# Kernel optimization log

Measured on AMD Instinct MI355X. Metric: run time of the kernel, lower is better.

## Reference

```python
import jax, jax.numpy as jnp
import numpy as np

ALPHA = 0.2  # LeakyReLU negative slope
NEG_INF = -9e15


def setup_inputs() -> dict:
    key = jax.random.key(0)
    k1, k2, k3, k4 = jax.random.split(key, 4)
    N, IN_F, OUT_F, H = 8192, 256, 128, 2
    HD = OUT_F // H
    h = jax.random.normal(k1, (N, IN_F), dtype=jnp.float32)
    adj = jax.random.randint(k2, (N, N), 0, 2, dtype=jnp.int32)
    # xavier_uniform with gain=1.414
    g = 1.414
    limW = g * np.sqrt(6.0 / (IN_F + HD))
    W = jax.random.uniform(k3, (H, IN_F, HD), jnp.float32, -limW, limW)
    lima = g * np.sqrt(6.0 / (2 * HD + 1))
    a = jax.random.uniform(k4, (H, 2 * HD, 1), jnp.float32, -lima, lima)
    return {"h": h, "adj": adj, "W": W, "a": a}


def reference(h, adj, W, a):
    # Wh: (H, N, HD)
    Wh = jnp.einsum('ni,hid->hnd', h, W)
    HD = W.shape[-1]
    a1 = a[:, :HD, 0]   # (H, HD) -> applied to Wh_i
    a2 = a[:, HD:, 0]   # (H, HD) -> applied to Wh_j
    # a . [Wh_i || Wh_j] == a1.Wh_i + a2.Wh_j ; avoids the (N,N,2HD) tensor
    f1 = jnp.einsum('hnd,hd->hn', Wh, a1)  # (H, N)
    f2 = jnp.einsum('hnd,hd->hn', Wh, a2)  # (H, N)
    e = jax.nn.leaky_relu(f1[:, :, None] + f2[:, None, :], ALPHA)  # (H, N, N)
    mask = (adj > 0)[None, :, :]
    e = jnp.where(mask, e, NEG_INF)
    attention = jax.nn.softmax(e, axis=-1)  # (H, N, N)
    # dropout is identity in eval mode
    h_prime = jnp.einsum('hnm,hmd->hnd', attention, Wh)  # (H, N, HD)
    N = h.shape[0]
    h_prime = jnp.transpose(h_prime, (1, 0, 2)).reshape(N, -1)  # concat heads
    return jax.nn.elu(h_prime)
```

## Files before the change

kernel.cpp:

```cpp
#include <hip/hip_runtime.h>
#include <hip/hip_bf16.h>
#include <stdint.h>

#define N_NODES 8192
#define IN_F    256
#define HD      64
#define NH      2
#define MS      8
#define SLICE   1024
#define NT      16
#define ALPHA   0.2f

typedef __attribute__((ext_vector_type(8))) short bf16x8s;
typedef __attribute__((ext_vector_type(4))) float f32x4;

#define OFF_U      0
#define OFF_WFRAG  4096
#define OFF_F1     69632
#define OFF_F2     135168
#define OFF_F2MAX  200704
#define OFF_G2     200960
#define OFF_WHB    332032
#define OFF_OP     2429184
#define OFF_LP     35983616

__device__ __forceinline__ unsigned short f2bf(float x) {
  union { float f; uint32_t u; } c; c.f = x;
  uint32_t r = c.u + 0x7FFFu + ((c.u >> 16) & 1u);
  return (unsigned short)(r >> 16);
}
__device__ __forceinline__ short f2bfs(float x) {
  __hip_bfloat16 b = __float2bfloat16(x);
  return __builtin_bit_cast(short, b);
}

__global__ void gat_prep_kernel(const float* __restrict__ W, const float* __restrict__ a,
                                float* __restrict__ u, unsigned short* __restrict__ wfrag)
{
  int idx = blockIdx.x * 256 + threadIdx.x;
  if (idx < 32768) {
    int j = idx & 7, lane = (idx >> 3) & 63, ks = (idx >> 9) & 7, Dt = idx >> 12;
    int k  = ks * 32 + ((lane >> 4) << 3) + j;
    int dp = Dt * 16 + (lane & 15);
    int hh = dp >> 6, d = dp & 63;
    wfrag[idx] = f2bf(W[(size_t)(hh * IN_F + k) * HD + d]);
  } else if (idx < 32768 + NH * 2 * IN_F) {
    int i2 = idx - 32768;
    int i = i2 & 255, v = (i2 >> 8) & 1, h = i2 >> 9;
    const float* Wp = W + (size_t)(h * IN_F + i) * HD;
    const float* ap = a + h * 2 * HD + v * HD;
    float s = 0.f;
    for (int d = 0; d < HD; ++d) s += Wp[d] * ap[d];
    u[(h * 2 + v) * IN_F + i] = s;
  }
}

__global__ __launch_bounds__(256) void gat_f12_kernel(const float* __restrict__ hmat,
    const float* __restrict__ u, float* __restrict__ f1, float* __restrict__ f2,
    uint32_t* __restrict__ g2b)
{
  int n = blockIdx.x * 4 + (threadIdx.x >> 6);
  int l = threadIdx.x & 63;
  float4 hv = *(const float4*)(hmat + (size_t)n * IN_F + l * 4);
  float s[4];
#pragma unroll
  for (int q = 0; q < 4; ++q) {
    float4 uv = *(const float4*)(u + q * IN_F + l * 4);
    s[q] = hv.x * uv.x + hv.y * uv.y + hv.z * uv.z + hv.w * uv.w;
  }
#pragma unroll
  for (int off = 1; off < 64; off <<= 1) {
#pragma unroll
    for (int q = 0; q < 4; ++q) s[q] += __shfl_xor(s[q], off);
  }
  if (l == 0) {
    f1[n] = s[0];           f2[n] = s[1];
    f1[N_NODES + n] = s[2]; f2[N_NODES + n] = s[3];
    g2b[n]           = (uint32_t)f2bf(__expf(s[1])) | ((uint32_t)f2bf(__expf(ALPHA * s[1])) << 16);
    g2b[N_NODES + n] = (uint32_t)f2bf(__expf(s[3])) | ((uint32_t)f2bf(__expf(ALPHA * s[3])) << 16);
  }
}

__global__ void gat_f2max_kernel(const float* __restrict__ f2, float* __restrict__ f2m)
{
  int h = blockIdx.x;
  float m = -1e30f;
  for (int i = threadIdx.x; i < N_NODES; i += 256) m = fmaxf(m, f2[h * N_NODES + i]);
#pragma unroll
  for (int off = 1; off < 64; off <<= 1) m = fmaxf(m, __shfl_xor(m, off));
  __shared__ float red[4];
  if ((threadIdx.x & 63) == 0) red[threadIdx.x >> 6] = m;
  __syncthreads();
  if (threadIdx.x == 0) f2m[h] = fmaxf(fmaxf(red[0], red[1]), fmaxf(red[2], red[3]));
}

__global__ __launch_bounds__(256) void gat_wh_kernel(const float* __restrict__ hmat,
    const unsigned short* __restrict__ wfrag, unsigned short* __restrict__ whb)
{
  int tid = threadIdx.x;
  int w = tid >> 6, l = tid & 63;
  int n0 = blockIdx.x * 64;
  int row = n0 + w * 16 + (l & 15);
  f32x4 acc[8] = {};
#pragma unroll
  for (int ks = 0; ks < 8; ++ks) {
    const float* ap = hmat + (size_t)row * IN_F + ks * 32 + ((l >> 4) << 3);
    float av[8];
    *(float4*)&av[0] = *(const float4*)ap;
    *(float4*)&av[4] = *(const float4*)(ap + 4);
    bf16x8s af;
#pragma unroll
    for (int j = 0; j < 8; ++j) af[j] = f2bfs(av[j]);
#pragma unroll
    for (int Dt = 0; Dt < 8; ++Dt) {
      bf16x8s bfv = *(const bf16x8s*)(wfrag + ((size_t)(Dt * 8 + ks) * 64 + l) * 8);
      acc[Dt] = __builtin_amdgcn_mfma_f32_16x16x32_bf16(af, bfv, acc[Dt], 0, 0, 0);
    }
  }
  int Tm = blockIdx.x;
  int s  = w >> 1;
  int lb = ((w & 1) * 2 + ((l >> 4) >> 1)) * 16 + (l & 15);
  int jh = (l >> 4) & 1;
#pragma unroll
  for (int Dt = 0; Dt < 8; ++Dt) {
    int hh = Dt >> 2, D = Dt & 3;
    ushort4 pk;
    pk.x = f2bf(acc[Dt][0]); pk.y = f2bf(acc[Dt][1]);
    pk.z = f2bf(acc[Dt][2]); pk.w = f2bf(acc[Dt][3]);
    size_t off = ((((size_t)(hh * 128 + Tm) * 2 + s) * 4 + D) * 64 + lb) * 8 + jh * 4;
    *(ushort4*)(whb + off) = pk;
  }
}

__global__ __launch_bounds__(256, 4) void gat_attn_kernel(
    const int* __restrict__ adj, const unsigned short* __restrict__ whb,
    const float* __restrict__ f1, const uint32_t* __restrict__ g2b,
    const float* __restrict__ f2max, float* __restrict__ Opart, float* __restrict__ Lpart)
{
  int bx = blockIdx.x;
  int split = bx & (MS - 1);
  int T = bx >> 3;
  int tid = threadIdx.x;
  int w = tid >> 6, l = tid & 63;
  int n0 = T * 64;
  int row = n0 + w * 16 + (l & 15);
  int mbase = split * SLICE;
  int koff = (l >> 4) << 3;
  int cb = mbase >> 6;

  __shared__ uint32_t glp[2][SLICE];
  __shared__ uint4 wbuf[2][1024];

  {
    const uint4* s0 = (const uint4*)(g2b + mbase);
    const uint4* s1 = (const uint4*)(g2b + N_NODES + mbase);
    ((uint4*)glp[0])[tid] = s0[tid];
    ((uint4*)glp[1])[tid] = s1[tid];
  }

  float E1[NH], Ea[NH];
#pragma unroll
  for (int h = 0; h < NH; ++h) {
    float f1v = f1[h * N_NODES + row];
    float tm  = f1v + f2max[h];
    float mrow = fmaxf(tm, ALPHA * tm);
    E1[h] = __expf(f1v - mrow);
    Ea[h] = __expf(ALPHA * f1v - mrow);
  }

  const int* ap = adj + (size_t)row * N_NODES + mbase + koff;
  const uint4* wsrc = (const uint4*)whb;

  uint4 rw0, rw1, rw2, rw3;
  {
    const uint4* w0 = wsrc + (size_t)cb * 512;
    const uint4* w1 = wsrc + (size_t)(128 + cb) * 512;
    rw0 = w0[tid]; rw1 = w0[tid + 256]; rw2 = w1[tid]; rw3 = w1[tid + 256];
  }
  int4 c0 = *(const int4*)(ap);      int4 c1 = *(const int4*)(ap + 4);
  int4 c2 = *(const int4*)(ap + 32); int4 c3 = *(const int4*)(ap + 36);
  wbuf[0][tid]       = rw0; wbuf[0][tid + 256] = rw1;
  wbuf[0][tid + 512] = rw2; wbuf[0][tid + 768] = rw3;
  __syncthreads();

  f32x4 acc[NH][4] = {};
  float lsum[NH] = {0.f, 0.f};

  for (int mt = 0; mt < NT; ++mt) {
    int p = mt & 1;
    if (mt + 1 < NT) {
      const uint4* w0 = wsrc + (size_t)(cb + mt + 1) * 512;
      const uint4* w1 = wsrc + (size_t)(128 + cb + mt + 1) * 512;
      rw0 = w0[tid]; rw1 = w0[tid + 256]; rw2 = w1[tid]; rw3 = w1[tid + 256];
    }

    bf16x8s af[NH][2];
#pragma unroll
    for (int s = 0; s < 2; ++s) {
      int aj[8];
      if (s == 0) { *(int4*)&aj[0] = c0; *(int4*)&aj[4] = c1; }
      else        { *(int4*)&aj[0] = c2; *(int4*)&aj[4] = c3; }
      uint32_t gv[NH][8];
#pragma unroll
      for (int h = 0; h < NH; ++h) {
        const uint4* gp = (const uint4*)&glp[h][mt * 64 + s * 32 + koff];
        *(uint4*)&gv[h][0] = gp[0];
        *(uint4*)&gv[h][4] = gp[1];
      }
#pragma unroll
      for (int h = 0; h < NH; ++h) {
        float ps = 0.f;
#pragma unroll
        for (int j = 0; j < 8; ++j) {
          uint32_t uv = gv[h][j];
          float g1 = __builtin_bit_cast(float, uv << 16);
          float ga = __builtin_bit_cast(float, uv & 0xffff0000u);
          float v  = fmaxf(E1[h] * g1, Ea[h] * ga);
          float pz = (aj[j] > 0) ? v : 0.f;
          ps += pz;
          af[h][s][j] = f2bfs(pz);
        }
        lsum[h] += ps;
      }
      if (mt + 1 < NT) {
        const int* apn = ap + (mt + 1) * 64;
        if (s == 0) { c0 = *(const int4*)(apn);      c1 = *(const int4*)(apn + 4); }
        else        { c2 = *(const int4*)(apn + 32); c3 = *(const int4*)(apn + 36); }
      }
    }

    const unsigned short* lb = (const unsigned short*)wbuf[p];
#pragma unroll
    for (int h = 0; h < NH; ++h)
#pragma unroll
      for (int s = 0; s < 2; ++s)
#pragma unroll
        for (int D = 0; D < 4; ++D) {
          bf16x8s bfv = *(const bf16x8s*)&lb[(h * 8 + s * 4 + D) * 512 + l * 8];
          acc[h][D] = __builtin_amdgcn_mfma_f32_16x16x32_bf16(af[h][s], bfv, acc[h][D], 0, 0, 0);
        }

    if (mt + 1 < NT) {
      wbuf[p ^ 1][tid]       = rw0; wbuf[p ^ 1][tid + 256] = rw1;
      wbuf[p ^ 1][tid + 512] = rw2; wbuf[p ^ 1][tid + 768] = rw3;
    }
    __syncthreads();
  }

#pragma unroll
  for (int h = 0; h < NH; ++h) {
    float ls = lsum[h];
    ls += __shfl_xor(ls, 16);
    ls += __shfl_xor(ls, 32);
    if (l < 16) Lpart[((size_t)(split * NH + h) << 13) + n0 + w * 16 + l] = ls;
    float* op = Opart + (size_t)(split * NH + h) * N_NODES * HD;
#pragma unroll
    for (int D = 0; D < 4; ++D)
#pragma unroll
      for (int r = 0; r < 4; ++r) {
        int orow = n0 + w * 16 + ((l >> 4) << 2) + r;
        op[(size_t)orow * HD + D * 16 + (l & 15)] = acc[h][D][r];
      }
  }
}

__global__ __launch_bounds__(256) void gat_final_kernel(const float* __restrict__ Opart,
    const float* __restrict__ Lpart, float* __restrict__ out)
{
  int idx = blockIdx.x * 256 + threadIdx.x;
  int n = idx >> 7, c = idx & 127;
  int h = c >> 6, d = c & 63;
  float v = 0.f, ls = 0.f;
#pragma unroll
  for (int sp = 0; sp < MS; ++sp) {
    v  += Opart[((size_t)(sp * NH + h) * N_NODES + n) * HD + d];
    ls += Lpart[(size_t)(sp * NH + h) * N_NODES + n];
  }
  float r = v / fmaxf(ls, 1e-30f);
  out[idx] = (r > 0.f) ? r : (__expf(r) - 1.f);
}

extern "C" void kernel_launch(void* const* d_in, const int* in_sizes, int n_in,
                              void* d_out, int out_size, void* d_ws, size_t ws_size,
                              hipStream_t stream)
{
  const float* hmat = (const float*)d_in[0];
  const int*   adj  = (const int*)d_in[1];
  const float* W    = (const float*)d_in[2];
  const float* a    = (const float*)d_in[3];
  float* out = (float*)d_out;
  char* ws = (char*)d_ws;

  float* u             = (float*)(ws + OFF_U);
  unsigned short* wfrg = (unsigned short*)(ws + OFF_WFRAG);
  float* f1            = (float*)(ws + OFF_F1);
  float* f2            = (float*)(ws + OFF_F2);
  float* f2m           = (float*)(ws + OFF_F2MAX);
  uint32_t* g2b        = (uint32_t*)(ws + OFF_G2);
  unsigned short* whb  = (unsigned short*)(ws + OFF_WHB);
  float* Opart         = (float*)(ws + OFF_OP);
  float* Lpart         = (float*)(ws + OFF_LP);

  gat_prep_kernel <<<132, 256, 0, stream>>>(W, a, u, wfrg);
  gat_f12_kernel  <<<N_NODES / 4, 256, 0, stream>>>(hmat, u, f1, f2, g2b);
  gat_f2max_kernel<<<NH, 256, 0, stream>>>(f2, f2m);
  gat_wh_kernel   <<<N_NODES / 64, 256, 0, stream>>>(hmat, wfrg, whb);
  gat_attn_kernel <<<128 * MS, 256, 0, stream>>>(adj, whb, f1, g2b, f2m, Opart, Lpart);
  gat_final_kernel<<<out_size / 256, 256, 0, stream>>>(Opart, Lpart, out);
}
```

Before: 113.2 us.

## Stage Wh tiles via direct global-to-LDS loads with triple buffering

```diff
diff --git a/kernel.cpp b/kernel.cpp
--- a/kernel.cpp
+++ b/kernel.cpp
@@ -13,6 +13,8 @@
 
 typedef __attribute__((ext_vector_type(8))) short bf16x8s;
 typedef __attribute__((ext_vector_type(4))) float f32x4;
+typedef __attribute__((address_space(3))) uint32_t lds_u32_t;
+typedef const __attribute__((address_space(1))) uint32_t gbl_u32_t;
 
 #define OFF_U      0
 #define OFF_WFRAG  4096
@@ -132,7 +134,7 @@
   }
 }
 
-__global__ __launch_bounds__(256, 4) void gat_attn_kernel(
+__global__ __launch_bounds__(256, 2) void gat_attn_kernel(
     const int* __restrict__ adj, const unsigned short* __restrict__ whb,
     const float* __restrict__ f1, const uint32_t* __restrict__ g2b,
     const float* __restrict__ f2max, float* __restrict__ Opart, float* __restrict__ Lpart)
@@ -149,7 +151,7 @@
   int cb = mbase >> 6;
 
   __shared__ uint32_t glp[2][SLICE];
-  __shared__ uint4 wbuf[2][1024];
+  __shared__ uint4 wbuf[3][1024];
 
   {
     const uint4* s0 = (const uint4*)(g2b + mbase);
@@ -168,51 +170,57 @@
     Ea[h] = __expf(ALPHA * f1v - mrow);
   }
 
+  __syncthreads();
+
   const int* ap = adj + (size_t)row * N_NODES + mbase + koff;
   const uint4* wsrc = (const uint4*)whb;
 
-  uint4 rw0, rw1, rw2, rw3;
-  {
-    const uint4* w0 = wsrc + (size_t)cb * 512;
-    const uint4* w1 = wsrc + (size_t)(128 + cb) * 512;
-    rw0 = w0[tid]; rw1 = w0[tid + 256]; rw2 = w1[tid]; rw3 = w1[tid + 256];
-  }
-  int4 c0 = *(const int4*)(ap);      int4 c1 = *(const int4*)(ap + 4);
-  int4 c2 = *(const int4*)(ap + 32); int4 c3 = *(const int4*)(ap + 36);
-  wbuf[0][tid]       = rw0; wbuf[0][tid + 256] = rw1;
-  wbuf[0][tid + 512] = rw2; wbuf[0][tid + 768] = rw3;
-  __syncthreads();
+  auto stage = [&](int tile, int bufi) {
+    const uint4* gsb = (w < 2)
+        ? (wsrc + (size_t)(cb + tile) * 512 + w * 256)
+        : (wsrc + (size_t)(128 + cb + tile) * 512 + (w - 2) * 256);
+    char* lb = (char*)&wbuf[0][0] + bufi * 16384 + w * 4096;
+#pragma unroll
+    for (int k = 0; k < 4; ++k) {
+      __builtin_amdgcn_global_load_lds((gbl_u32_t*)(gsb + k * 64 + l),
+                                       (lds_u32_t*)(lb + k * 1024), 16, 0, 0);
+    }
+  };
+  auto ldadj = [&](int tile, int4* c) {
+    const int* p = ap + tile * 64;
+    c[0] = *(const int4*)p;        c[1] = *(const int4*)(p + 4);
+    c[2] = *(const int4*)(p + 32); c[3] = *(const int4*)(p + 36);
+  };
+
+  int4 cE[4], cO[4];
+  stage(0, 0); ldadj(0, cE);
+  stage(1, 1); ldadj(1, cO);
 
   f32x4 acc[NH][4] = {};
   float lsum[NH] = {0.f, 0.f};
 
-  for (int mt = 0; mt < NT; ++mt) {
-    int p = mt & 1;
-    if (mt + 1 < NT) {
-      const uint4* w0 = wsrc + (size_t)(cb + mt + 1) * 512;
-      const uint4* w1 = wsrc + (size_t)(128 + cb + mt + 1) * 512;
-      rw0 = w0[tid]; rw1 = w0[tid + 256]; rw2 = w1[tid]; rw3 = w1[tid + 256];
-    }
+  auto body = [&](int mt, int4* cc) {
+    if (mt < NT - 1) asm volatile("s_waitcnt vmcnt(8)" ::: "memory");
+    else             asm volatile("s_waitcnt vmcnt(0)" ::: "memory");
+    __builtin_amdgcn_s_barrier();
+
+    int cur = mt % 3;
 
     bf16x8s af[NH][2];
 #pragma unroll
     for (int s = 0; s < 2; ++s) {
       int aj[8];
-      if (s == 0) { *(int4*)&aj[0] = c0; *(int4*)&aj[4] = c1; }
-      else        { *(int4*)&aj[0] = c2; *(int4*)&aj[4] = c3; }
-      uint32_t gv[NH][8];
+      *(int4*)&aj[0] = cc[2 * s]; *(int4*)&aj[4] = cc[2 * s + 1];
 #pragma unroll
       for (int h = 0; h < NH; ++h) {
         const uint4* gp = (const uint4*)&glp[h][mt * 64 + s * 32 + koff];
-        *(uint4*)&gv[h][0] = gp[0];
-        *(uint4*)&gv[h][4] = gp[1];
-      }
-#pragma unroll
-      for (int h = 0; h < NH; ++h) {
+        uint32_t gv[8];
+        *(uint4*)&gv[0] = gp[0];
+        *(uint4*)&gv[4] = gp[1];
         float ps = 0.f;
 #pragma unroll
         for (int j = 0; j < 8; ++j) {
-          uint32_t uv = gv[h][j];
+          uint32_t uv = gv[j];
           float g1 = __builtin_bit_cast(float, uv << 16);
           float ga = __builtin_bit_cast(float, uv & 0xffff0000u);
           float v  = fmaxf(E1[h] * g1, Ea[h] * ga);
@@ -222,14 +230,14 @@
         }
         lsum[h] += ps;
       }
-      if (mt + 1 < NT) {
-        const int* apn = ap + (mt + 1) * 64;
-        if (s == 0) { c0 = *(const int4*)(apn);      c1 = *(const int4*)(apn + 4); }
-        else        { c2 = *(const int4*)(apn + 32); c3 = *(const int4*)(apn + 36); }
-      }
     }
 
-    const unsigned short* lb = (const unsigned short*)wbuf[p];
+    if (mt + 2 < NT) {
+      stage(mt + 2, (mt + 2) % 3);
+      ldadj(mt + 2, cc);
+    }
+
+    const unsigned short* lb = (const unsigned short*)wbuf + (size_t)cur * 8192;
 #pragma unroll
     for (int h = 0; h < NH; ++h)
 #pragma unroll
@@ -239,12 +247,11 @@
           bf16x8s bfv = *(const bf16x8s*)&lb[(h * 8 + s * 4 + D) * 512 + l * 8];
           acc[h][D] = __builtin_amdgcn_mfma_f32_16x16x32_bf16(af[h][s], bfv, acc[h][D], 0, 0, 0);
         }
-
-    if (mt + 1 < NT) {
-      wbuf[p ^ 1][tid]       = rw0; wbuf[p ^ 1][tid + 256] = rw1;
-      wbuf[p ^ 1][tid + 512] = rw2; wbuf[p ^ 1][tid + 768] = rw3;
-    }
-    __syncthreads();
+  };
+
+  for (int mt = 0; mt < NT; mt += 2) {
+    body(mt, cE);
+    body(mt + 1, cO);
   }
 
 #pragma unroll
```

Result: slower. 118.3 us (+4.5%).

## Bitpack adjacency in LDS, split columns across waves, fuse final reduction

Applied to the files above, without the earlier changes.

```diff
diff --git a/kernel.cpp b/kernel.cpp
--- a/kernel.cpp
+++ b/kernel.cpp
@@ -6,9 +6,7 @@
 #define IN_F    256
 #define HD      64
 #define NH      2
-#define MS      8
-#define SLICE   1024
-#define NT      16
+#define BROWS   32
 #define ALPHA   0.2f
 
 typedef __attribute__((ext_vector_type(8))) short bf16x8s;
@@ -21,8 +19,6 @@
 #define OFF_F2MAX  200704
 #define OFF_G2     200960
 #define OFF_WHB    332032
-#define OFF_OP     2429184
-#define OFF_LP     35983616
 
 __device__ __forceinline__ unsigned short f2bf(float x) {
   union { float f; uint32_t u; } c; c.f = x;
@@ -132,152 +128,172 @@
   }
 }
 
-__global__ __launch_bounds__(256, 4) void gat_attn_kernel(
+__global__ __launch_bounds__(512, 2) void gat_attn_kernel(
     const int* __restrict__ adj, const unsigned short* __restrict__ whb,
     const float* __restrict__ f1, const uint32_t* __restrict__ g2b,
-    const float* __restrict__ f2max, float* __restrict__ Opart, float* __restrict__ Lpart)
-{
-  int bx = blockIdx.x;
-  int split = bx & (MS - 1);
-  int T = bx >> 3;
+    const float* __restrict__ f2max, float* __restrict__ out)
+{
+  __shared__ unsigned long long maskbuf[BROWS][128];
+  __shared__ uint32_t glp[2][N_NODES];
+  __shared__ float redbuf[12288];
+  __shared__ float lsumbuf[8][2][16];
+
   int tid = threadIdx.x;
-  int w = tid >> 6, l = tid & 63;
-  int n0 = T * 64;
-  int row = n0 + w * 16 + (l & 15);
-  int mbase = split * SLICE;
+  int wv = tid >> 6, l = tid & 63;
+  int rb = blockIdx.x * BROWS;
+
+  {
+    uint4* gd = (uint4*)glp;
+    const uint4* gs = (const uint4*)g2b;
+#pragma unroll
+    for (int i = 0; i < 8; ++i) gd[i * 512 + tid] = gs[i * 512 + tid];
+  }
+
+#pragma unroll 1
+  for (int r = 0; r < 4; ++r) {
+    int lrow = wv * 4 + r;
+    const int4* src = (const int4*)(adj + (size_t)(rb + lrow) * N_NODES) + l;
+#pragma unroll 1
+    for (int cc = 0; cc < 4; ++cc) {
+      int4 v[8];
+#pragma unroll
+      for (int u2 = 0; u2 < 8; ++u2) v[u2] = src[(cc * 8 + u2) * 64];
+#pragma unroll
+      for (int u2 = 0; u2 < 8; ++u2) {
+        int c = cc * 8 + u2;
+        unsigned long long b0 = __ballot(v[u2].x > 0);
+        unsigned long long b1 = __ballot(v[u2].y > 0);
+        unsigned long long b2 = __ballot(v[u2].z > 0);
+        unsigned long long b3 = __ballot(v[u2].w > 0);
+        if (l == 0) {
+          ulonglong2* mp = (ulonglong2*)&maskbuf[lrow][c * 4];
+          mp[0] = make_ulonglong2(b0, b1);
+          mp[1] = make_ulonglong2(b2, b3);
+        }
+      }
+    }
+  }
+  __syncthreads();
+
+  int h = wv & 1, q = wv >> 1;
+  int mtbase = q * 32;
   int koff = (l >> 4) << 3;
-  int cb = mbase >> 6;
-
-  __shared__ uint32_t glp[2][SLICE];
-  __shared__ uint4 wbuf[2][1024];
-
-  {
-    const uint4* s0 = (const uint4*)(g2b + mbase);
-    const uint4* s1 = (const uint4*)(g2b + N_NODES + mbase);
-    ((uint4*)glp[0])[tid] = s0[tid];
-    ((uint4*)glp[1])[tid] = s1[tid];
-  }
-
-  float E1[NH], Ea[NH];
-#pragma unroll
-  for (int h = 0; h < NH; ++h) {
-    float f1v = f1[h * N_NODES + row];
+
+  float E1v[2], Eav[2];
+#pragma unroll
+  for (int rg = 0; rg < 2; ++rg) {
+    float f1v = f1[h * N_NODES + rb + rg * 16 + (l & 15)];
     float tm  = f1v + f2max[h];
     float mrow = fmaxf(tm, ALPHA * tm);
-    E1[h] = __expf(f1v - mrow);
-    Ea[h] = __expf(ALPHA * f1v - mrow);
-  }
-
-  const int* ap = adj + (size_t)row * N_NODES + mbase + koff;
-  const uint4* wsrc = (const uint4*)whb;
-
-  uint4 rw0, rw1, rw2, rw3;
-  {
-    const uint4* w0 = wsrc + (size_t)cb * 512;
-    const uint4* w1 = wsrc + (size_t)(128 + cb) * 512;
-    rw0 = w0[tid]; rw1 = w0[tid + 256]; rw2 = w1[tid]; rw3 = w1[tid + 256];
-  }
-  int4 c0 = *(const int4*)(ap);      int4 c1 = *(const int4*)(ap + 4);
-  int4 c2 = *(const int4*)(ap + 32); int4 c3 = *(const int4*)(ap + 36);
-  wbuf[0][tid]       = rw0; wbuf[0][tid + 256] = rw1;
-  wbuf[0][tid + 512] = rw2; wbuf[0][tid + 768] = rw3;
-  __syncthreads();
-
-  f32x4 acc[NH][4] = {};
-  float lsum[NH] = {0.f, 0.f};
-
-  for (int mt = 0; mt < NT; ++mt) {
-    int p = mt & 1;
-    if (mt + 1 < NT) {
-      const uint4* w0 = wsrc + (size_t)(cb + mt + 1) * 512;
-      const uint4* w1 = wsrc + (size_t)(128 + cb + mt + 1) * 512;
-      rw0 = w0[tid]; rw1 = w0[tid + 256]; rw2 = w1[tid]; rw3 = w1[tid + 256];
-    }
-
-    bf16x8s af[NH][2];
+    E1v[rg] = __expf(f1v - mrow);
+    Eav[rg] = __expf(ALPHA * f1v - mrow);
+  }
+
+  const uint4* wp = (const uint4*)whb + ((size_t)(h * 128 + mtbase) * 8) * 64 + l;
+
+  f32x4 acc[2][4] = {};
+  float lsum[2] = {0.f, 0.f};
+  unsigned long long cm[2][4];
+  uint4 cur[8], nxt[8];
+#pragma unroll
+  for (int i = 0; i < 8; ++i) cur[i] = wp[i * 64];
+
+#pragma unroll 2
+  for (int t = 0; t < 32; ++t) {
+    int mt = mtbase + t;
+    if ((t & 3) == 0) {
+      int cidx = (mt >> 2) * 4;
+      ulonglong2 m00 = *(const ulonglong2*)&maskbuf[l & 15][cidx];
+      ulonglong2 m01 = *(const ulonglong2*)&maskbuf[l & 15][cidx + 2];
+      ulonglong2 m10 = *(const ulonglong2*)&maskbuf[16 + (l & 15)][cidx];
+      ulonglong2 m11 = *(const ulonglong2*)&maskbuf[16 + (l & 15)][cidx + 2];
+      cm[0][0] = m00.x; cm[0][1] = m00.y; cm[0][2] = m01.x; cm[0][3] = m01.y;
+      cm[1][0] = m10.x; cm[1][1] = m10.y; cm[1][2] = m11.x; cm[1][3] = m11.y;
+    }
+    if (t + 1 < 32) {
+      const uint4* p = wp + (size_t)(t + 1) * 512;
+#pragma unroll
+      for (int i = 0; i < 8; ++i) nxt[i] = p[i * 64];
+    }
+
+    bf16x8s af[2][2];
 #pragma unroll
     for (int s = 0; s < 2; ++s) {
-      int aj[8];
-      if (s == 0) { *(int4*)&aj[0] = c0; *(int4*)&aj[4] = c1; }
-      else        { *(int4*)&aj[0] = c2; *(int4*)&aj[4] = c3; }
-      uint32_t gv[NH][8];
-#pragma unroll
-      for (int h = 0; h < NH; ++h) {
-        const uint4* gp = (const uint4*)&glp[h][mt * 64 + s * 32 + koff];
-        *(uint4*)&gv[h][0] = gp[0];
-        *(uint4*)&gv[h][4] = gp[1];
-      }
-#pragma unroll
-      for (int h = 0; h < NH; ++h) {
+      int sh = ((mt & 3) << 4) + (s << 3) + ((l >> 4) << 1);
+      const uint4* gp = (const uint4*)&glp[h][(mt << 6) + s * 32 + koff];
+      uint32_t gv[8];
+      *(uint4*)&gv[0] = gp[0];
+      *(uint4*)&gv[4] = gp[1];
+#pragma unroll
+      for (int rg = 0; rg < 2; ++rg) {
+        uint32_t b0 = (uint32_t)(cm[rg][0] >> sh), b1 = (uint32_t)(cm[rg][1] >> sh);
+        uint32_t b2 = (uint32_t)(cm[rg][2] >> sh), b3 = (uint32_t)(cm[rg][3] >> sh);
         float ps = 0.f;
 #pragma unroll
         for (int j = 0; j < 8; ++j) {
-          uint32_t uv = gv[h][j];
+          uint32_t uv = gv[j];
           float g1 = __builtin_bit_cast(float, uv << 16);
           float ga = __builtin_bit_cast(float, uv & 0xffff0000u);
-          float v  = fmaxf(E1[h] * g1, Ea[h] * ga);
-          float pz = (aj[j] > 0) ? v : 0.f;
-          ps += pz;
-          af[h][s][j] = f2bfs(pz);
+          float v  = fmaxf(E1v[rg] * g1, Eav[rg] * ga);
+          uint32_t bb = (j & 3) == 0 ? b0 : (j & 3) == 1 ? b1 : (j & 3) == 2 ? b2 : b3;
+          float p = ((bb >> (j >> 2)) & 1) ? v : 0.f;
+          ps += p;
+          af[rg][s][j] = f2bfs(p);
         }
-        lsum[h] += ps;
+        lsum[rg] += ps;
       }
-      if (mt + 1 < NT) {
-        const int* apn = ap + (mt + 1) * 64;
-        if (s == 0) { c0 = *(const int4*)(apn);      c1 = *(const int4*)(apn + 4); }
-        else        { c2 = *(const int4*)(apn + 32); c3 = *(const int4*)(apn + 36); }
+    }
+
+#pragma unroll
+    for (int s = 0; s < 2; ++s)
+#pragma unroll
+      for (int D = 0; D < 4; ++D) {
+        bf16x8s bfv = __builtin_bit_cast(bf16x8s, cur[s * 4 + D]);
+        acc[0][D] = __builtin_amdgcn_mfma_f32_16x16x32_bf16(af[0][s], bfv, acc[0][D], 0, 0, 0);
+        acc[1][D] = __builtin_amdgcn_mfma_f32_16x16x32_bf16(af[1][s], bfv, acc[1][D], 0, 0, 0);
       }
-    }
-
-    const unsigned short* lb = (const unsigned short*)wbuf[p];
-#pragma unroll
-    for (int h = 0; h < NH; ++h)
-#pragma unroll
-      for (int s = 0; s < 2; ++s)
-#pragma unroll
-        for (int D = 0; D < 4; ++D) {
-          bf16x8s bfv = *(const bf16x8s*)&lb[(h * 8 + s * 4 + D) * 512 + l * 8];
-          acc[h][D] = __builtin_amdgcn_mfma_f32_16x16x32_bf16(af[h][s], bfv, acc[h][D], 0, 0, 0);
-        }
-
-    if (mt + 1 < NT) {
-      wbuf[p ^ 1][tid]       = rw0; wbuf[p ^ 1][tid + 256] = rw1;
-      wbuf[p ^ 1][tid + 512] = rw2; wbuf[p ^ 1][tid + 768] = rw3;
-    }
-    __syncthreads();
-  }
-
-#pragma unroll
-  for (int h = 0; h < NH; ++h) {
-    float ls = lsum[h];
+#pragma unroll
+    for (int i = 0; i < 8; ++i) cur[i] = nxt[i];
+  }
+
+#pragma unroll
+  for (int rg = 0; rg < 2; ++rg) {
+    float ls = lsum[rg];
     ls += __shfl_xor(ls, 16);
     ls += __shfl_xor(ls, 32);
-    if (l < 16) Lpart[((size_t)(split * NH + h) << 13) + n0 + w * 16 + l] = ls;
-    float* op = Opart + (size_t)(split * NH + h) * N_NODES * HD;
-#pragma unroll
-    for (int D = 0; D < 4; ++D)
-#pragma unroll
-      for (int r = 0; r < 4; ++r) {
-        int orow = n0 + w * 16 + ((l >> 4) << 2) + r;
-        op[(size_t)orow * HD + D * 16 + (l & 15)] = acc[h][D][r];
-      }
-  }
-}
-
-__global__ __launch_bounds__(256) void gat_final_kernel(const float* __restrict__ Opart,
-    const float* __restrict__ Lpart, float* __restrict__ out)
-{
-  int idx = blockIdx.x * 256 + threadIdx.x;
-  int n = idx >> 7, c = idx & 127;
-  int h = c >> 6, d = c & 63;
-  float v = 0.f, ls = 0.f;
-#pragma unroll
-  for (int sp = 0; sp < MS; ++sp) {
-    v  += Opart[((size_t)(sp * NH + h) * N_NODES + n) * HD + d];
-    ls += Lpart[(size_t)(sp * NH + h) * N_NODES + n];
-  }
-  float r = v / fmaxf(ls, 1e-30f);
-  out[idx] = (r > 0.f) ? r : (__expf(r) - 1.f);
+    if (l < 16) lsumbuf[wv][rg][l] = ls;
+  }
+  __syncthreads();
+
+  if (q > 0) {
+    float* rp = &redbuf[(h * 3 + (q - 1)) * 2048];
+#pragma unroll
+    for (int rg = 0; rg < 2; ++rg)
+#pragma unroll
+      for (int D = 0; D < 4; ++D)
+#pragma unroll
+        for (int r = 0; r < 4; ++r)
+          rp[rg * 1024 + D * 256 + ((l >> 4) * 4 + r) * 16 + (l & 15)] = acc[rg][D][r];
+  }
+  __syncthreads();
+  if (q == 0) {
+    const float* rp = &redbuf[h * 3 * 2048];
+#pragma unroll
+    for (int rg = 0; rg < 2; ++rg)
+#pragma unroll
+      for (int D = 0; D < 4; ++D)
+#pragma unroll
+        for (int r = 0; r < 4; ++r) {
+          int rr = (l >> 4) * 4 + r;
+          int ri = rg * 1024 + D * 256 + rr * 16 + (l & 15);
+          float v = acc[rg][D][r] + rp[ri] + rp[2048 + ri] + rp[4096 + ri];
+          float ls = lsumbuf[h][rg][rr] + lsumbuf[2 + h][rg][rr]
+                   + lsumbuf[4 + h][rg][rr] + lsumbuf[6 + h][rg][rr];
+          float o = v / fmaxf(ls, 1e-30f);
+          out[(size_t)(rb + rg * 16 + rr) * (NH * HD) + h * HD + D * 16 + (l & 15)]
+              = (o > 0.f) ? o : (__expf(o) - 1.f);
+        }
+  }
 }
 
 extern "C" void kernel_launch(void* const* d_in, const int* in_sizes, int n_in,
@@ -298,13 +314,10 @@
   float* f2m           = (float*)(ws + OFF_F2MAX);
   uint32_t* g2b        = (uint32_t*)(ws + OFF_G2);
   unsigned short* whb  = (unsigned short*)(ws + OFF_WHB);
-  float* Opart         = (float*)(ws + OFF_OP);
-  float* Lpart         = (float*)(ws + OFF_LP);
 
   gat_prep_kernel <<<132, 256, 0, stream>>>(W, a, u, wfrg);
   gat_f12_kernel  <<<N_NODES / 4, 256, 0, stream>>>(hmat, u, f1, f2, g2b);
   gat_f2max_kernel<<<NH, 256, 0, stream>>>(f2, f2m);
   gat_wh_kernel   <<<N_NODES / 64, 256, 0, stream>>>(hmat, wfrg, whb);
-  gat_attn_kernel <<<128 * MS, 256, 0, stream>>>(adj, whb, f1, g2b, f2m, Opart, Lpart);
-  gat_final_kernel<<<out_size / 256, 256, 0, stream>>>(Opart, Lpart, out);
-}
+  gat_attn_kernel <<<N_NODES / BROWS, 512, 0, stream>>>(adj, whb, f1, g2b, f2m, out);
+}
```

After: 121.1 us. 1.07x slower.
